# Kernel optimization log

Hardware: AMD Instinct MI355X
Metric: run time of the kernel (lower is better)

Reference implementation:

```python
import jax, jax.numpy as jnp
import numpy as np

EMB = 768
HEADS = 8
HEAD_DIM = EMB // HEADS  # 96


def setup_inputs() -> dict:
    key = jax.random.key(0)
    ks = jax.random.split(key, 9)
    B, S = 16, 1024
    s = 1.0 / np.sqrt(EMB)
    inp = {
        "input_embeddings": jax.random.normal(ks[0], (B, S, EMB), dtype=jnp.float32),
        "Wq": jax.random.normal(ks[1], (EMB, EMB), dtype=jnp.float32) * s,
        "bq": jnp.zeros((EMB,), dtype=jnp.float32),
        "Wk": jax.random.normal(ks[2], (EMB, EMB), dtype=jnp.float32) * s,
        "bk": jnp.zeros((EMB,), dtype=jnp.float32),
        "Wv": jax.random.normal(ks[3], (EMB, EMB), dtype=jnp.float32) * s,
        "bv": jnp.zeros((EMB,), dtype=jnp.float32),
        "Wo": jax.random.normal(ks[4], (EMB, EMB), dtype=jnp.float32) * s,
        "bo": jnp.zeros((EMB,), dtype=jnp.float32),
    }
    return inp


def reference(input_embeddings, Wq, bq, Wk, bk, Wv, bv, Wo, bo):
    B, S, _ = input_embeddings.shape
    # QKV projections (torch Linear: x @ W.T + b; here W stored as [in,out])
    q = input_embeddings @ Wq + bq
    k = input_embeddings @ Wk + bk
    v = input_embeddings @ Wv + bv
    # [B, H, S, Dh]
    q = q.reshape(B, S, HEADS, HEAD_DIM).transpose(0, 2, 1, 3)
    k = k.reshape(B, S, HEADS, HEAD_DIM).transpose(0, 2, 1, 3)
    v = v.reshape(B, S, HEADS, HEAD_DIM).transpose(0, 2, 1, 3)
    scores = jnp.einsum("bhqd,bhkd->bhqk", q, k) / np.sqrt(HEAD_DIM)
    probs = jax.nn.softmax(scores, axis=-1)  # dropout=0 (eval)
    context = jnp.einsum("bhqk,bhkd->bhqd", probs, v)
    context = context.transpose(0, 2, 1, 3).reshape(B, S, HEADS * HEAD_DIM)
    output = context @ Wo + bo
    return (output, probs)
```

## Files before the change

kernel.cpp:

```cpp
#include <hip/hip_runtime.h>

typedef _Float16 half8 __attribute__((ext_vector_type(8)));
typedef _Float16 half4 __attribute__((ext_vector_type(4)));
typedef float f32x4 __attribute__((ext_vector_type(4)));

__device__ __forceinline__ void lds_load16(const void* g, void* l) {
  __builtin_amdgcn_global_load_lds((const __attribute__((address_space(1))) void*)g,
                                   (__attribute__((address_space(3))) void*)l, 16, 0, 0);
}

__global__ __launch_bounds__(256) void cvt_x(const float* __restrict__ in,
                                             _Float16* __restrict__ out) {
  int i = blockIdx.x * 256 + threadIdx.x;
  const float4* p = (const float4*)(in + (size_t)i * 8);
  float4 a = p[0], b = p[1];
  half8 v;
  v[0] = (_Float16)a.x; v[1] = (_Float16)a.y; v[2] = (_Float16)a.z; v[3] = (_Float16)a.w;
  v[4] = (_Float16)b.x; v[5] = (_Float16)b.y; v[6] = (_Float16)b.z; v[7] = (_Float16)b.w;
  *(half8*)(out + (size_t)i * 8) = v;
}

__global__ __launch_bounds__(256) void cvt_w(const float* __restrict__ Wq, const float* __restrict__ Wk,
                                             const float* __restrict__ Wv, const float* __restrict__ Wo,
                                             _Float16* __restrict__ Wqkvt, _Float16* __restrict__ Wot) {
  int id = blockIdx.x * 256 + threadIdx.x;
  int part = id / 589824;
  int r = id - part * 589824;
  int k = r / 768;
  int n = r - k * 768;
  const float* W = part == 0 ? Wq : part == 1 ? Wk : part == 2 ? Wv : Wo;
  _Float16 v = (_Float16)W[(size_t)k * 768 + n];
  if (part < 3) Wqkvt[((size_t)(part * 768 + n)) * 768 + k] = v;
  else          Wot[(size_t)n * 768 + k] = v;
}

template <int EPI>
__global__ __launch_bounds__(256) void gemm_f16(
    const _Float16* __restrict__ A, const _Float16* __restrict__ Bt,
    const float* __restrict__ b0, const float* __restrict__ b1, const float* __restrict__ b2,
    _Float16* __restrict__ Qo, _Float16* __restrict__ Ko, _Float16* __restrict__ Vto,
    float* __restrict__ Co) {
  const int K = 768;
  __shared__ _Float16 As[128 * 32];
  __shared__ _Float16 Bs[128 * 32];
  const int tid = threadIdx.x, w = tid >> 6, l = tid & 63;
  const int lr = l & 15, lk = l >> 4;
  const int m0 = blockIdx.y * 128, n0 = blockIdx.x * 128;
  const int wr = w >> 1, wc = w & 1;
  f32x4 acc[4][4] = {};
  const int arow = tid >> 2;
  const int acolb = (tid & 3) * 16;

  for (int k0 = 0; k0 < K; k0 += 32) {
    __syncthreads();
#pragma unroll
    for (int c = 0; c < 2; ++c) {
      lds_load16((const char*)(A + (size_t)(m0 + c * 64 + arow) * K + k0) + acolb,
                 (char*)As + c * 4096 + w * 1024);
      lds_load16((const char*)(Bt + (size_t)(n0 + c * 64 + arow) * K + k0) + acolb,
                 (char*)Bs + c * 4096 + w * 1024);
    }
    __syncthreads();
    half8 af[4], bf[4];
#pragma unroll
    for (int mi = 0; mi < 4; ++mi) af[mi] = *(const half8*)&As[(wr * 64 + mi * 16 + lr) * 32 + lk * 8];
#pragma unroll
    for (int ni = 0; ni < 4; ++ni) bf[ni] = *(const half8*)&Bs[(wc * 64 + ni * 16 + lr) * 32 + lk * 8];
#pragma unroll
    for (int mi = 0; mi < 4; ++mi)
#pragma unroll
      for (int ni = 0; ni < 4; ++ni)
        acc[mi][ni] = __builtin_amdgcn_mfma_f32_16x16x32_f16(af[mi], bf[ni], acc[mi][ni], 0, 0, 0);
  }

#pragma unroll
  for (int mi = 0; mi < 4; ++mi) {
    const int rbase = m0 + wr * 64 + mi * 16 + lk * 4;
#pragma unroll
    for (int ni = 0; ni < 4; ++ni) {
      const int col = n0 + wc * 64 + ni * 16 + lr;
      if (EPI == 0) {
        const int part = col / 768;
        const int e = col - part * 768;
        const int h = e / 96, d = e - (e / 96) * 96;
        const float* bb = part == 0 ? b0 : part == 1 ? b1 : b2;
        const float bv = bb[e];
#pragma unroll
        for (int j = 0; j < 4; ++j) {
          const int row = rbase + j;
          const int b = row >> 10, s = row & 1023;
          const int bh = b * 8 + h;
          const _Float16 v = (_Float16)(acc[mi][ni][j] + bv);
          if (part < 2) {
            const size_t idx = ((((size_t)(bh * 64 + (s >> 4)) * 3 + (d >> 5)) * 64
                                + ((d & 31) >> 3) * 16 + (s & 15)) << 3) + (d & 7);
            if (part == 0) Qo[idx] = v; else Ko[idx] = v;
          } else {
            const size_t idx = ((((size_t)(bh * 6 + (d >> 4)) * 32 + (s >> 5)) * 64
                                + ((s & 31) >> 3) * 16 + (d & 15)) << 3) + (s & 7);
            Vto[idx] = v;
          }
        }
      } else {
        const float bv = b0[col];
#pragma unroll
        for (int j = 0; j < 4; ++j) {
          const int row = rbase + j;
          Co[(size_t)row * 768 + col] = acc[mi][ni][j] + bv;
        }
      }
    }
  }
}

__global__ __launch_bounds__(512, 2) void attn(const _Float16* __restrict__ swzQ,
                                               const _Float16* __restrict__ swzK,
                                               const _Float16* __restrict__ swzV,
                                               float* __restrict__ probs,
                                               _Float16* __restrict__ ctx) {
  __shared__ __align__(16) float Pf[8][16][132];
  __shared__ float lsb[8][2][16];
  const int tid = threadIdx.x, w = tid >> 6, l = tid & 63;
  const int lr = l & 15, lk = l >> 4;
  const int id = blockIdx.x;
  const int lid = (id & 7) * 512 + (id >> 3);
  const int bh = lid >> 5, qt2 = lid & 31;
  const int q0 = qt2 * 32;
  const float SC = 0.10206207261596577f * 1.4426950408889634f;
  const int b = bh >> 3, h = bh & 7;

  const half8* qbA = (const half8*)swzQ + (size_t)(bh * 64 + qt2 * 2) * 192;
  const half8* kb  = (const half8*)swzK + (size_t)(bh * 64 + w * 8) * 192;
  const half8* vb0 = (const half8*)swzV + (size_t)bh * 12288;
  half8 bqA[3], bqB[3];
#pragma unroll
  for (int kk = 0; kk < 3; ++kk) { bqA[kk] = qbA[kk * 64 + l]; bqB[kk] = qbA[192 + kk * 64 + l]; }
  half8 kf[8][3];
#pragma unroll
  for (int ct = 0; ct < 8; ++ct)
#pragma unroll
    for (int kk = 0; kk < 3; ++kk) kf[ct][kk] = kb[(ct * 3 + kk) * 64 + l];

  f32x4 sA[8], sB[8];
#pragma unroll
  for (int ct = 0; ct < 8; ++ct) {
    f32x4 aA = {0.f, 0.f, 0.f, 0.f}, aB = {0.f, 0.f, 0.f, 0.f};
#pragma unroll
    for (int kk = 0; kk < 3; ++kk) {
      aA = __builtin_amdgcn_mfma_f32_16x16x32_f16(kf[ct][kk], bqA[kk], aA, 0, 0, 0);
      aB = __builtin_amdgcn_mfma_f32_16x16x32_f16(kf[ct][kk], bqB[kk], aB, 0, 0, 0);
    }
    sA[ct] = aA; sB[ct] = aB;
  }

  float psA = 0.f, psB = 0.f;
#pragma unroll
  for (int ct = 0; ct < 8; ++ct)
#pragma unroll
    for (int j = 0; j < 4; ++j) {
      const float eA = __builtin_amdgcn_exp2f(sA[ct][j] * SC);
      const float eB = __builtin_amdgcn_exp2f(sB[ct][j] * SC);
      sA[ct][j] = eA; psA += eA;
      sB[ct][j] = eB; psB += eB;
    }
  psA += __shfl_xor(psA, 16); psA += __shfl_xor(psA, 32);
  psB += __shfl_xor(psB, 16); psB += __shfl_xor(psB, 32);
  if (lk == 0) { lsb[w][0][lr] = psA; lsb[w][1][lr] = psB; }

  half8 vf[6][4];
#pragma unroll
  for (int dt = 0; dt < 6; ++dt)
#pragma unroll
    for (int kk = 0; kk < 4; ++kk) vf[dt][kk] = vb0[(dt * 32 + w * 4 + kk) * 64 + l];

  __syncthreads();
  float ltA = 0.f, ltB = 0.f;
#pragma unroll
  for (int ww = 0; ww < 8; ++ww) { ltA += lsb[ww][0][lr]; ltB += lsb[ww][1][lr]; }
  const float invlA = 1.f / ltA, invlB = 1.f / ltB;

  const int qh = l >> 5, c4 = (l & 31) * 4;
  float* cbw = (float*)&Pf[w][0][0];
  const int rq = tid >> 5;
  const int rd0 = (tid & 31) * 3;

#pragma unroll
  for (int ct = 0; ct < 8; ++ct) {
    f32x4 p4;
#pragma unroll
    for (int j = 0; j < 4; ++j) p4[j] = sA[ct][j] * invlA;
    *(f32x4*)&Pf[w][lr][ct * 16 + lk * 4] = p4;
  }
  {
    float* pbase = probs + ((size_t)bh << 20) + (size_t)q0 * 1024 + w * 128;
#pragma unroll
    for (int r2 = 0; r2 < 8; ++r2) {
      const int q = r2 * 2 + qh;
      f32x4 v = *(const f32x4*)&Pf[w][q][c4];
      __builtin_nontemporal_store(v, (f32x4*)(pbase + (size_t)q * 1024 + c4));
    }
  }
  f32x4 cacc[6] = {};
#pragma unroll
  for (int kk = 0; kk < 4; ++kk) {
    f32x4 a0 = *(const f32x4*)&Pf[w][lr][kk * 32 + lk * 8];
    f32x4 a1 = *(const f32x4*)&Pf[w][lr][kk * 32 + lk * 8 + 4];
    half8 pa;
#pragma unroll
    for (int e = 0; e < 4; ++e) { pa[e] = (_Float16)a0[e]; pa[4 + e] = (_Float16)a1[e]; }
#pragma unroll
    for (int dt = 0; dt < 6; ++dt)
      cacc[dt] = __builtin_amdgcn_mfma_f32_16x16x32_f16(pa, vf[dt][kk], cacc[dt], 0, 0, 0);
  }
#pragma unroll
  for (int dt = 0; dt < 6; ++dt)
#pragma unroll
    for (int j = 0; j < 4; ++j)
      cbw[(lk * 4 + j) * 100 + dt * 16 + lr] = cacc[dt][j];
  __syncthreads();
  {
    _Float16* cg = ctx + ((size_t)(b * 1024 + q0 + rq)) * 768 + h * 96 + rd0;
#pragma unroll
    for (int e = 0; e < 3; ++e) {
      float v = 0.f;
#pragma unroll
      for (int ww = 0; ww < 8; ++ww) v += ((const float*)&Pf[ww][0][0])[rq * 100 + rd0 + e];
      cg[e] = (_Float16)v;
    }
  }
  __syncthreads();

#pragma unroll
  for (int ct = 0; ct < 8; ++ct) {
    f32x4 p4;
#pragma unroll
    for (int j = 0; j < 4; ++j) p4[j] = sB[ct][j] * invlB;
    *(f32x4*)&Pf[w][lr][ct * 16 + lk * 4] = p4;
  }
  {
    float* pbase = probs + ((size_t)bh << 20) + (size_t)(q0 + 16) * 1024 + w * 128;
#pragma unroll
    for (int r2 = 0; r2 < 8; ++r2) {
      const int q = r2 * 2 + qh;
      f32x4 v = *(const f32x4*)&Pf[w][q][c4];
      __builtin_nontemporal_store(v, (f32x4*)(pbase + (size_t)q * 1024 + c4));
    }
  }
#pragma unroll
  for (int dt = 0; dt < 6; ++dt) cacc[dt] = f32x4{0.f, 0.f, 0.f, 0.f};
#pragma unroll
  for (int kk = 0; kk < 4; ++kk) {
    f32x4 a0 = *(const f32x4*)&Pf[w][lr][kk * 32 + lk * 8];
    f32x4 a1 = *(const f32x4*)&Pf[w][lr][kk * 32 + lk * 8 + 4];
    half8 pa;
#pragma unroll
    for (int e = 0; e < 4; ++e) { pa[e] = (_Float16)a0[e]; pa[4 + e] = (_Float16)a1[e]; }
#pragma unroll
    for (int dt = 0; dt < 6; ++dt)
      cacc[dt] = __builtin_amdgcn_mfma_f32_16x16x32_f16(pa, vf[dt][kk], cacc[dt], 0, 0, 0);
  }
#pragma unroll
  for (int dt = 0; dt < 6; ++dt)
#pragma unroll
    for (int j = 0; j < 4; ++j)
      cbw[(lk * 4 + j) * 100 + dt * 16 + lr] = cacc[dt][j];
  __syncthreads();
  {
    _Float16* cg = ctx + ((size_t)(b * 1024 + q0 + 16 + rq)) * 768 + h * 96 + rd0;
#pragma unroll
    for (int e = 0; e < 3; ++e) {
      float v = 0.f;
#pragma unroll
      for (int ww = 0; ww < 8; ++ww) v += ((const float*)&Pf[ww][0][0])[rq * 100 + rd0 + e];
      cg[e] = (_Float16)v;
    }
  }
}

extern "C" void kernel_launch(void* const* d_in, const int* in_sizes, int n_in,
                              void* d_out, int out_size, void* d_ws, size_t ws_size,
                              hipStream_t stream) {
  (void)in_sizes; (void)n_in; (void)out_size; (void)ws_size;
  const float* X  = (const float*)d_in[0];
  const float* Wq = (const float*)d_in[1];
  const float* bq = (const float*)d_in[2];
  const float* Wk = (const float*)d_in[3];
  const float* bk = (const float*)d_in[4];
  const float* Wv = (const float*)d_in[5];
  const float* bv = (const float*)d_in[6];
  const float* Wo = (const float*)d_in[7];
  const float* bo = (const float*)d_in[8];

  char* ws = (char*)d_ws;
  _Float16* Xh    = (_Float16*)(ws + 0);
  _Float16* Wqkvt = (_Float16*)(ws + 25165824);
  _Float16* Wot   = (_Float16*)(ws + 28704768);
  _Float16* Qh    = (_Float16*)(ws + 29884416);
  _Float16* Kh    = (_Float16*)(ws + 55050240);
  _Float16* Vth   = (_Float16*)(ws + 80216064);
  _Float16* Ctx   = (_Float16*)(ws + 105381888);

  float* out   = (float*)d_out;
  float* probs = out + 12582912;

  cvt_x<<<dim3(6144), dim3(256), 0, stream>>>(X, Xh);
  cvt_w<<<dim3(9216), dim3(256), 0, stream>>>(Wq, Wk, Wv, Wo, Wqkvt, Wot);
  gemm_f16<0><<<dim3(18, 128), dim3(256), 0, stream>>>(Xh, Wqkvt, bq, bk, bv, Qh, Kh, Vth, nullptr);
  attn<<<dim3(4096), dim3(512), 0, stream>>>(Qh, Kh, Vth, probs, Ctx);
  gemm_f16<1><<<dim3(6, 128), dim3(256), 0, stream>>>(Ctx, Wot, bo, bo, bo, nullptr, nullptr, nullptr, out);
}
```

Before: 328.1 us.

## Replace GEMMs with 256x256-tile double-buffered LDS pipeline and XCD-aware block mapping

Rewrites both projection GEMMs to use 256x256 output tiles with 512 threads, a K-step of 64, and double-buffered LDS staging so global loads for the next tile overlap MFMA work on the current one. Blocks are remapped across the eight XCDs, MFMA sections get raised wave priority, and the output projection uses nontemporal stores. The larger tiles improve operand reuse and cut barrier overhead, but they raise LDS and register use, and the output GEMM now launches fewer blocks than there are CUs.

```diff
diff --git a/kernel.cpp b/kernel.cpp
--- a/kernel.cpp
+++ b/kernel.cpp
@@ -34,51 +34,77 @@
   else          Wot[(size_t)n * 768 + k] = v;
 }
 
-template <int EPI>
-__global__ __launch_bounds__(256) void gemm_f16(
+template <int EPI, int NB>
+__global__ __launch_bounds__(512, 2) void gemm256(
     const _Float16* __restrict__ A, const _Float16* __restrict__ Bt,
     const float* __restrict__ b0, const float* __restrict__ b1, const float* __restrict__ b2,
     _Float16* __restrict__ Qo, _Float16* __restrict__ Ko, _Float16* __restrict__ Vto,
     float* __restrict__ Co) {
-  const int K = 768;
-  __shared__ _Float16 As[128 * 32];
-  __shared__ _Float16 Bs[128 * 32];
+  __shared__ _Float16 Ab[2 * 16384];
+  __shared__ _Float16 Bb[2 * 16384];
   const int tid = threadIdx.x, w = tid >> 6, l = tid & 63;
   const int lr = l & 15, lk = l >> 4;
-  const int m0 = blockIdx.y * 128, n0 = blockIdx.x * 128;
-  const int wr = w >> 1, wc = w & 1;
-  f32x4 acc[4][4] = {};
-  const int arow = tid >> 2;
-  const int acolb = (tid & 3) * 16;
-
-  for (int k0 = 0; k0 < K; k0 += 32) {
-    __syncthreads();
-#pragma unroll
-    for (int c = 0; c < 2; ++c) {
-      lds_load16((const char*)(A + (size_t)(m0 + c * 64 + arow) * K + k0) + acolb,
-                 (char*)As + c * 4096 + w * 1024);
-      lds_load16((const char*)(Bt + (size_t)(n0 + c * 64 + arow) * K + k0) + acolb,
-                 (char*)Bs + c * 4096 + w * 1024);
-    }
-    __syncthreads();
-    half8 af[4], bf[4];
-#pragma unroll
-    for (int mi = 0; mi < 4; ++mi) af[mi] = *(const half8*)&As[(wr * 64 + mi * 16 + lr) * 32 + lk * 8];
-#pragma unroll
-    for (int ni = 0; ni < 4; ++ni) bf[ni] = *(const half8*)&Bs[(wc * 64 + ni * 16 + lr) * 32 + lk * 8];
-#pragma unroll
-    for (int mi = 0; mi < 4; ++mi)
-#pragma unroll
-      for (int ni = 0; ni < 4; ++ni)
-        acc[mi][ni] = __builtin_amdgcn_mfma_f32_16x16x32_f16(af[mi], bf[ni], acc[mi][ni], 0, 0, 0);
-  }
-
-#pragma unroll
-  for (int mi = 0; mi < 4; ++mi) {
-    const int rbase = m0 + wr * 64 + mi * 16 + lk * 4;
+  const int wm = w >> 2, wn = w & 3;
+  const int q8 = (int)gridDim.x >> 3;
+  const int wg = ((int)blockIdx.x & 7) * q8 + ((int)blockIdx.x >> 3);
+  const int m0 = (wg / NB) * 256, n0 = (wg % NB) * 256;
+
+  const int srow = tid >> 3;
+  const int scol = (tid & 7) * 8;
+
+  auto STAGE = [&](int kt, int dstb) {
+#pragma unroll
+    for (int c = 0; c < 4; ++c) {
+      lds_load16(A + (size_t)(m0 + c * 64 + srow) * 768 + kt * 64 + scol,
+                 (char*)Ab + dstb * 32768 + c * 8192 + tid * 16);
+      lds_load16(Bt + (size_t)(n0 + c * 64 + srow) * 768 + kt * 64 + scol,
+                 (char*)Bb + dstb * 32768 + c * 8192 + tid * 16);
+    }
+  };
+
+  f32x4 acc[8][4] = {};
+  STAGE(0, 0);
+
+  for (int T = 0; T < 12; ++T) {
+    const int b = T & 1;
+    asm volatile("s_waitcnt vmcnt(0)" ::: "memory");
+    asm volatile("s_barrier" ::: "memory");
+    if (T < 11) STAGE(T + 1, b ^ 1);
+    const _Float16* Ax = Ab + b * 16384;
+    const _Float16* Bx = Bb + b * 16384;
+    half8 bf[4][2];
+#pragma unroll
+    for (int ni = 0; ni < 4; ++ni)
+#pragma unroll
+      for (int ks = 0; ks < 2; ++ks)
+        bf[ni][ks] = *(const half8*)&Bx[(wn * 64 + ni * 16 + lr) * 64 + ks * 32 + lk * 8];
+#pragma unroll
+    for (int qd = 0; qd < 4; ++qd) {
+      half8 af[2][2];
+#pragma unroll
+      for (int i = 0; i < 2; ++i)
+#pragma unroll
+        for (int ks = 0; ks < 2; ++ks)
+          af[i][ks] = *(const half8*)&Ax[(wm * 128 + (qd * 2 + i) * 16 + lr) * 64 + ks * 32 + lk * 8];
+      __builtin_amdgcn_s_setprio(1);
+#pragma unroll
+      for (int i = 0; i < 2; ++i)
+#pragma unroll
+        for (int ni = 0; ni < 4; ++ni)
+#pragma unroll
+          for (int ks = 0; ks < 2; ++ks)
+            acc[qd * 2 + i][ni] =
+                __builtin_amdgcn_mfma_f32_16x16x32_f16(af[i][ks], bf[ni][ks], acc[qd * 2 + i][ni], 0, 0, 0);
+      __builtin_amdgcn_s_setprio(0);
+    }
+  }
+
+#pragma unroll
+  for (int mi = 0; mi < 8; ++mi) {
+    const int rbase = m0 + wm * 128 + mi * 16 + lk * 4;
 #pragma unroll
     for (int ni = 0; ni < 4; ++ni) {
-      const int col = n0 + wc * 64 + ni * 16 + lr;
+      const int col = n0 + wn * 64 + ni * 16 + lr;
       if (EPI == 0) {
         const int part = col / 768;
         const int e = col - part * 768;
@@ -88,8 +114,8 @@
 #pragma unroll
         for (int j = 0; j < 4; ++j) {
           const int row = rbase + j;
-          const int b = row >> 10, s = row & 1023;
-          const int bh = b * 8 + h;
+          const int bI = row >> 10, s = row & 1023;
+          const int bh = bI * 8 + h;
           const _Float16 v = (_Float16)(acc[mi][ni][j] + bv);
           if (part < 2) {
             const size_t idx = ((((size_t)(bh * 64 + (s >> 4)) * 3 + (d >> 5)) * 64
@@ -106,7 +132,7 @@
 #pragma unroll
         for (int j = 0; j < 4; ++j) {
           const int row = rbase + j;
-          Co[(size_t)row * 768 + col] = acc[mi][ni][j] + bv;
+          __builtin_nontemporal_store(acc[mi][ni][j] + bv, Co + (size_t)row * 768 + col);
         }
       }
     }
@@ -305,7 +331,7 @@
 
   cvt_x<<<dim3(6144), dim3(256), 0, stream>>>(X, Xh);
   cvt_w<<<dim3(9216), dim3(256), 0, stream>>>(Wq, Wk, Wv, Wo, Wqkvt, Wot);
-  gemm_f16<0><<<dim3(18, 128), dim3(256), 0, stream>>>(Xh, Wqkvt, bq, bk, bv, Qh, Kh, Vth, nullptr);
+  gemm256<0, 9><<<dim3(576), dim3(512), 0, stream>>>(Xh, Wqkvt, bq, bk, bv, Qh, Kh, Vth, nullptr);
   attn<<<dim3(4096), dim3(512), 0, stream>>>(Qh, Kh, Vth, probs, Ctx);
-  gemm_f16<1><<<dim3(6, 128), dim3(256), 0, stream>>>(Ctx, Wot, bo, bo, bo, nullptr, nullptr, nullptr, out);
-}
+  gemm256<1, 3><<<dim3(192), dim3(512), 0, stream>>>(Ctx, Wot, bo, bo, bo, nullptr, nullptr, nullptr, out);
+}
```

After: 341.1 us. 1.04x slower.

## Double-buffer GEMM LDS tiles with XOR swizzle and XCD-aware block remap

Applied to the files above, without the earlier changes.

Rewrites both projection GEMMs to double-buffer the LDS tiles, so the next K-tile's global-to-LDS load is issued while MFMAs run on the current one. The tile layout uses an XOR swizzle to cut LDS bank conflicts, and blocks are remapped across XCDs for cache locality. It also raises MFMA priority, sets launch bounds to 4 blocks per CU, and uses nontemporal stores for the fp32 output. The cost is twice the LDS per block and a hand-written waitcnt/barrier sequence that must stay correct.

```diff
diff --git a/kernel.cpp b/kernel.cpp
--- a/kernel.cpp
+++ b/kernel.cpp
@@ -34,51 +34,68 @@
   else          Wot[(size_t)n * 768 + k] = v;
 }
 
-template <int EPI>
-__global__ __launch_bounds__(256) void gemm_f16(
+template <int EPI, int NB>
+__global__ __launch_bounds__(256, 4) void gemm128(
     const _Float16* __restrict__ A, const _Float16* __restrict__ Bt,
     const float* __restrict__ b0, const float* __restrict__ b1, const float* __restrict__ b2,
     _Float16* __restrict__ Qo, _Float16* __restrict__ Ko, _Float16* __restrict__ Vto,
     float* __restrict__ Co) {
-  const int K = 768;
-  __shared__ _Float16 As[128 * 32];
-  __shared__ _Float16 Bs[128 * 32];
+  __shared__ _Float16 Ab[2][128 * 32];
+  __shared__ _Float16 Bb[2][128 * 32];
   const int tid = threadIdx.x, w = tid >> 6, l = tid & 63;
   const int lr = l & 15, lk = l >> 4;
-  const int m0 = blockIdx.y * 128, n0 = blockIdx.x * 128;
-  const int wr = w >> 1, wc = w & 1;
+  const int wm = w >> 1, wn = w & 1;
+  const int q8 = (int)gridDim.x >> 3;
+  const int wg = ((int)blockIdx.x & 7) * q8 + ((int)blockIdx.x >> 3);
+  const int m0 = (wg / NB) * 128, n0 = (wg % NB) * 128;
+
+  const int r0 = (tid >> 2);
+
+  auto STAGE = [&](int kt, int dstb) {
+#pragma unroll
+    for (int i = 0; i < 2; ++i) {
+      const int g = i * 256 + tid;
+      const int row = g >> 2;
+      const int gr = (g & 3) ^ (row & 3);
+      lds_load16(A + (size_t)(m0 + row) * 768 + kt * 32 + gr * 8,
+                 (char*)&Ab[dstb][0] + g * 16);
+      lds_load16(Bt + (size_t)(n0 + row) * 768 + kt * 32 + gr * 8,
+                 (char*)&Bb[dstb][0] + g * 16);
+    }
+  };
+  (void)r0;
+
   f32x4 acc[4][4] = {};
-  const int arow = tid >> 2;
-  const int acolb = (tid & 3) * 16;
-
-  for (int k0 = 0; k0 < K; k0 += 32) {
-    __syncthreads();
-#pragma unroll
-    for (int c = 0; c < 2; ++c) {
-      lds_load16((const char*)(A + (size_t)(m0 + c * 64 + arow) * K + k0) + acolb,
-                 (char*)As + c * 4096 + w * 1024);
-      lds_load16((const char*)(Bt + (size_t)(n0 + c * 64 + arow) * K + k0) + acolb,
-                 (char*)Bs + c * 4096 + w * 1024);
-    }
-    __syncthreads();
+  STAGE(0, 0);
+  const int swzg = ((lk ^ (lr & 3)) * 8);
+
+  for (int T = 0; T < 24; ++T) {
+    const int b = T & 1;
+    asm volatile("s_waitcnt vmcnt(0)" ::: "memory");
+    asm volatile("s_barrier" ::: "memory");
+    if (T < 23) STAGE(T + 1, b ^ 1);
     half8 af[4], bf[4];
 #pragma unroll
-    for (int mi = 0; mi < 4; ++mi) af[mi] = *(const half8*)&As[(wr * 64 + mi * 16 + lr) * 32 + lk * 8];
-#pragma unroll
-    for (int ni = 0; ni < 4; ++ni) bf[ni] = *(const half8*)&Bs[(wc * 64 + ni * 16 + lr) * 32 + lk * 8];
+    for (int mi = 0; mi < 4; ++mi)
+      af[mi] = *(const half8*)&Ab[b][(wm * 64 + mi * 16 + lr) * 32 + swzg];
+#pragma unroll
+    for (int ni = 0; ni < 4; ++ni)
+      bf[ni] = *(const half8*)&Bb[b][(wn * 64 + ni * 16 + lr) * 32 + swzg];
+    __builtin_amdgcn_s_setprio(1);
 #pragma unroll
     for (int mi = 0; mi < 4; ++mi)
 #pragma unroll
       for (int ni = 0; ni < 4; ++ni)
         acc[mi][ni] = __builtin_amdgcn_mfma_f32_16x16x32_f16(af[mi], bf[ni], acc[mi][ni], 0, 0, 0);
+    __builtin_amdgcn_s_setprio(0);
   }
 
 #pragma unroll
   for (int mi = 0; mi < 4; ++mi) {
-    const int rbase = m0 + wr * 64 + mi * 16 + lk * 4;
+    const int rbase = m0 + wm * 64 + mi * 16 + lk * 4;
 #pragma unroll
     for (int ni = 0; ni < 4; ++ni) {
-      const int col = n0 + wc * 64 + ni * 16 + lr;
+      const int col = n0 + wn * 64 + ni * 16 + lr;
       if (EPI == 0) {
         const int part = col / 768;
         const int e = col - part * 768;
@@ -88,8 +105,8 @@
 #pragma unroll
         for (int j = 0; j < 4; ++j) {
           const int row = rbase + j;
-          const int b = row >> 10, s = row & 1023;
-          const int bh = b * 8 + h;
+          const int bI = row >> 10, s = row & 1023;
+          const int bh = bI * 8 + h;
           const _Float16 v = (_Float16)(acc[mi][ni][j] + bv);
           if (part < 2) {
             const size_t idx = ((((size_t)(bh * 64 + (s >> 4)) * 3 + (d >> 5)) * 64
@@ -106,7 +123,7 @@
 #pragma unroll
         for (int j = 0; j < 4; ++j) {
           const int row = rbase + j;
-          Co[(size_t)row * 768 + col] = acc[mi][ni][j] + bv;
+          __builtin_nontemporal_store(acc[mi][ni][j] + bv, Co + (size_t)row * 768 + col);
         }
       }
     }
@@ -305,7 +322,7 @@
 
   cvt_x<<<dim3(6144), dim3(256), 0, stream>>>(X, Xh);
   cvt_w<<<dim3(9216), dim3(256), 0, stream>>>(Wq, Wk, Wv, Wo, Wqkvt, Wot);
-  gemm_f16<0><<<dim3(18, 128), dim3(256), 0, stream>>>(Xh, Wqkvt, bq, bk, bv, Qh, Kh, Vth, nullptr);
+  gemm128<0, 18><<<dim3(2304), dim3(256), 0, stream>>>(Xh, Wqkvt, bq, bk, bv, Qh, Kh, Vth, nullptr);
   attn<<<dim3(4096), dim3(512), 0, stream>>>(Qh, Kh, Vth, probs, Ctx);
-  gemm_f16<1><<<dim3(6, 128), dim3(256), 0, stream>>>(Ctx, Wot, bo, bo, bo, nullptr, nullptr, nullptr, out);
-}
+  gemm128<1, 6><<<dim3(768), dim3(256), 0, stream>>>(Ctx, Wot, bo, bo, bo, nullptr, nullptr, nullptr, out);
+}
```

After: 307.9 us. 6.1% less time.
